# Optimization experiments

Hardware: AMD Instinct MI355X
Metric: run time of the kernel (lower is better)

The kernel has to match this reference:

```python
import jax, jax.numpy as jnp
import numpy as np

D = 64          # hidden_size
NU = 32768      # num user nodes
NI = 16384      # num item nodes
DEG = 50        # mailbox degree (== user_max_length == item_max_length)


def setup_inputs() -> dict:
    key = jax.random.key(0)
    ks = jax.random.split(key, 14)
    s = 1.0 / np.sqrt(D)
    return {
        'user_feat': jax.random.normal(ks[0], (NU, D), jnp.float32),
        'item_feat': jax.random.normal(ks[1], (NI, D), jnp.float32),
        'W_user': jax.random.normal(ks[2], (D, D), jnp.float32) * s,
        'W_item': jax.random.normal(ks[3], (D, D), jnp.float32) * s,
        'gate_u': jax.random.normal(ks[4], (D, 2 * D), jnp.float32) * s,
        'gate_i': jax.random.normal(ks[5], (D, 2 * D), jnp.float32) * s,
        'u_te': jax.random.normal(ks[6], (DEG, D), jnp.float32),
        'u_te_k': jax.random.normal(ks[7], (DEG, D), jnp.float32),
        'i_te': jax.random.normal(ks[8], (DEG, D), jnp.float32),
        'i_te_k': jax.random.normal(ks[9], (DEG, D), jnp.float32),
        'user_nbr': jax.random.randint(ks[10], (NU, DEG), 0, NI, jnp.int32),
        'item_nbr': jax.random.randint(ks[11], (NI, DEG), 0, NU, jnp.int32),
        'user_time': jax.random.randint(ks[12], (NU, DEG), 0, 1000000, jnp.int32),
        'item_time': jax.random.randint(ks[13], (NI, DEG), 0, 1000000, jnp.int32),
    }


def _orgat_att_agg(mail, dst_h, times, te, te_k, gate):
    """One reduce_func: 'orgat' long-term + 'att' short-term, gated concat.
    mail: [N, K, D] neighbor (src) embeddings; dst_h: [N, D]; times: [N, K] int.
    """
    k = times.shape[1]
    # rank of each time within the mailbox, then reversed order index
    order = jnp.argsort(jnp.argsort(times, axis=1), axis=1)
    re_order = k - order - 1                              # [N, K] in [0, K)
    scale = jnp.sqrt(jnp.asarray(mail.shape[-1], mail.dtype))
    # long-term: time-aware attention against dst embedding
    e = jnp.einsum('nkd,nd->nk', te[re_order] + mail, dst_h) / scale
    alpha = jax.nn.softmax(e, axis=1)
    h_long = jnp.einsum('nk,nkd->nd', alpha, mail + te_k[re_order])
    # short-term: attention against most-recent neighbor embedding
    last = jnp.argmax(times, axis=1)                      # [N]
    last_em = jnp.take_along_axis(mail, last[:, None, None], axis=1)[:, 0]
    e1 = jnp.einsum('nkd,nd->nk', mail, last_em) / scale
    alpha1 = jax.nn.softmax(e1, axis=1)
    h_short = jnp.einsum('nk,nkd->nd', alpha1, mail)
    return jnp.concatenate([h_long, h_short], axis=-1) @ gate.T


def reference(user_feat, item_feat, W_user, W_item, gate_u, gate_i,
              u_te, u_te_k, i_te, i_te_k,
              user_nbr, item_nbr, user_time, item_time):
    # linear projections (dropout disabled / eval mode)
    user_h = user_feat @ W_user.T
    item_h = item_feat @ W_item.T
    # item nodes aggregate from neighboring users ('by' relation)
    item_mail = user_h[item_nbr]                          # [NI, DEG, D] gather
    item_new = _orgat_att_agg(item_mail, item_h, item_time, i_te, i_te_k, gate_i)
    # user nodes aggregate from neighboring items ('pby' relation)
    user_mail = item_h[user_nbr]                          # [NU, DEG, D] gather
    user_new = _orgat_att_agg(user_mail, user_h, user_time, u_te, u_te_k, gate_u)
    # residual update with ELU against the pre-projection features
    user_out = jax.nn.elu(user_new + user_feat)
    item_out = jax.nn.elu(item_new + item_feat)
    return user_out, item_out
```

## Files before the change

### kernel.cpp

```cpp
#include <hip/hip_runtime.h>
#include <math.h>

#define NU 32768
#define NI 16384
#define DH 64
#define KK 50

typedef unsigned short ushort_t;
typedef __attribute__((ext_vector_type(8))) short  bf16x8;
typedef __attribute__((ext_vector_type(4))) float  f32x4;
typedef __attribute__((ext_vector_type(4))) unsigned int u32x4;

__device__ __forceinline__ unsigned cvtpk(float lo, float hi) {
    unsigned r;
    asm("v_cvt_pk_bf16_f32 %0, %1, %2" : "=v"(r) : "v"(lo), "v"(hi));
    return r;
}
__device__ __forceinline__ bf16x8 as_bf(u32x4 v) {
    union { u32x4 u; bf16x8 b; } x; x.u = v; return x.b;
}
__device__ __forceinline__ ushort_t bf16r(float v) {
    unsigned u = __float_as_uint(v);
    u += 0x7fffu + ((u >> 16) & 1u);
    return (ushort_t)(u >> 16);
}
__device__ __forceinline__ u32x4 pk8(const float* p) {
    float4 a = *(const float4*)p;
    float4 b = *(const float4*)(p + 4);
    u32x4 r;
    r[0] = cvtpk(a.x, a.y); r[1] = cvtpk(a.z, a.w);
    r[2] = cvtpk(b.x, b.y); r[3] = cvtpk(b.z, b.w);
    return r;
}

__global__ __launch_bounds__(256) void projprep_kernel(
    const float* __restrict__ user_feat, const float* __restrict__ item_feat,
    const float* __restrict__ W_user,    const float* __restrict__ W_item,
    const float* __restrict__ gate_u,    const float* __restrict__ gate_i,
    const float* __restrict__ u_te,      const float* __restrict__ i_te,
    const float* __restrict__ u_te_k,    const float* __restrict__ i_te_k,
    ushort_t* __restrict__ hbf_u, ushort_t* __restrict__ hbf_i,
    ushort_t* __restrict__ teA_u, ushort_t* __restrict__ teA_i,
    ushort_t* __restrict__ gA_u,  ushort_t* __restrict__ gA_i)
{
    __shared__ __align__(16) float SH[3200];
    const int b    = blockIdx.x;
    const int tid  = threadIdx.x;
    const int w    = tid >> 6;
    const int lane = tid & 63;
    const int c = lane & 15, g = lane >> 4;

    if (b < 768) {
        const bool isU = b < 512;
        const float* feat = isU ? user_feat : item_feat;
        const float* W    = isU ? W_user    : W_item;
        ushort_t*    hbf  = isU ? hbf_u     : hbf_i;
        const int    bb   = isU ? b : b - 512;

        ushort_t* WA = (ushort_t*)SH;
        for (int i = tid; i < 4096; i += 256) {
            int j = i & 7, l = (i >> 3) & 63, s = (i >> 9) & 1, mt = i >> 10;
            int row = mt * 16 + (l & 15);
            int k   = s * 32 + ((l >> 4) & 3) * 8 + j;
            WA[i] = bf16r(W[row * DH + k]);
        }
        __syncthreads();

        const int nb = bb * 64 + w * 16;
        u32x4 bf[2];
        #pragma unroll
        for (int s = 0; s < 2; ++s)
            bf[s] = pk8(feat + (size_t)(nb + c) * DH + s * 32 + g * 8);

        #pragma unroll
        for (int mt = 0; mt < 4; ++mt) {
            f32x4 acc = {0.f, 0.f, 0.f, 0.f};
            #pragma unroll
            for (int s = 0; s < 2; ++s) {
                u32x4 af = *(const u32x4*)(WA + ((mt * 2 + s) * 64 + lane) * 8);
                acc = __builtin_amdgcn_mfma_f32_16x16x32_bf16(as_bf(af), as_bf(bf[s]), acc, 0, 0, 0);
            }
            uint2 p;
            p.x = cvtpk(acc[0], acc[1]);
            p.y = cvtpk(acc[2], acc[3]);
            *(uint2*)(hbf + (size_t)(nb + c) * DH + mt * 16 + g * 4) = p;
        }
    } else {
        const int rel = b - 768;
        const float* gate = rel ? gate_i : gate_u;
        const float* te   = rel ? i_te   : u_te;
        const float* tek  = rel ? i_te_k : u_te_k;
        ushort_t* teA = rel ? teA_i : teA_u;
        ushort_t* gA  = rel ? gA_i  : gA_u;
        float* M = SH;

        {
            const int d = w * 16 + c;
            u32x4 ga[2];
            #pragma unroll
            for (int s = 0; s < 2; ++s)
                ga[s] = pk8(gate + (size_t)d * 128 + s * 32 + g * 8);
            #pragma unroll
            for (int rt = 0; rt < 4; ++rt) {
                int r = rt * 16 + c;
                const float* tr = tek + (size_t)(r < KK ? r : 0) * DH;
                f32x4 acc = {0.f, 0.f, 0.f, 0.f};
                #pragma unroll
                for (int s = 0; s < 2; ++s) {
                    u32x4 bfr = pk8(tr + s * 32 + g * 8);
                    acc = __builtin_amdgcn_mfma_f32_16x16x32_bf16(as_bf(ga[s]), as_bf(bfr), acc, 0, 0, 0);
                }
                if (r < KK) {
                    #pragma unroll
                    for (int jj = 0; jj < 4; ++jj)
                        M[(w * 16 + g * 4 + jj) * KK + r] = acc[jj];
                }
            }
        }
        __syncthreads();

        for (int i = tid; i < 4096; i += 256) {
            int j = i & 7, l = (i >> 3) & 63, s = (i >> 9) & 1, t = i >> 10;
            int r = t * 16 + (l & 15);
            int d = s * 32 + ((l >> 4) & 3) * 8 + j;
            teA[i] = bf16r(r < KK ? te[r * DH + d] : 0.f);
        }
        for (int i = tid; i < 12288; i += 256) {
            int j = i & 7, l = (i >> 3) & 63, q = i >> 9;
            int s = q % 6, mt = q / 6;
            int d = mt * 16 + (l & 15);
            int k = s * 32 + ((l >> 4) & 3) * 8 + j;
            float v = 0.f;
            if (k < 128)            v = gate[d * 128 + k];
            else if (k < 128 + KK)  v = M[d * KK + (k - 128)];
            gA[i] = bf16r(v);
        }
    }
}

__global__ __launch_bounds__(128) void agg_kernel(
    const ushort_t* __restrict__ h_src,
    const ushort_t* __restrict__ h_dst,
    const int*      __restrict__ nbr,
    const int*      __restrict__ times,
    const ushort_t* __restrict__ teA,
    ushort_t*       __restrict__ ccout)
{
    __shared__ __align__(16) float EBs[2][192];

    const int wid  = threadIdx.x >> 6;
    const int lane = threadIdx.x & 63;
    const int n    = blockIdx.x * 2 + wid;

    float* EB = EBs[wid];
    const int c = lane & 15;
    const int g = lane >> 4;

    int my_t = 0, my_nb = 0;
    if (lane < KK) {
        my_t  = times[n * KK + lane];
        my_nb = nbr[n * KK + lane];
    }

    u32x4 af[4][2];
    #pragma unroll
    for (int t = 0; t < 4; ++t) {
        int r = t * 16 + c;
        int idx = __builtin_amdgcn_ds_bpermute(r << 2, my_nb);
        const ushort_t* src = h_src + idx * DH;
        #pragma unroll
        for (int s = 0; s < 2; ++s)
            af[t][s] = *(const u32x4*)(src + s * 32 + g * 8);
    }

    int key = my_t * 64 + lane;
    int sro = 0;
    #pragma unroll
    for (int j = 0; j < KK; ++j) {
        int kj = __builtin_amdgcn_readlane(key, j);
        sro += (kj > key) ? 1 : 0;
    }

    int key2 = (lane < KK) ? (my_t * 64 + (63 - lane)) : -1;
    #pragma unroll
    for (int off = 32; off >= 1; off >>= 1) {
        int o = __shfl_xor(key2, off);
        key2 = key2 > o ? key2 : o;
    }
    const int last   = __builtin_amdgcn_readfirstlane(63 - (key2 & 63));
    const int t_last = last >> 4;
    const int c_last = last & 15;

    u32x4 fbv[2];
    {
        const ushort_t* hd = h_dst + n * DH;
        u32x4 sl0, sl1;
        if      (t_last == 0) { sl0 = af[0][0]; sl1 = af[0][1]; }
        else if (t_last == 1) { sl0 = af[1][0]; sl1 = af[1][1]; }
        else if (t_last == 2) { sl0 = af[2][0]; sl1 = af[2][1]; }
        else                  { sl0 = af[3][0]; sl1 = af[3][1]; }
        const int ba = ((lane & 48) + c_last) << 2;
        const bool is1 = (c == 1);
        #pragma unroll
        for (int s = 0; s < 2; ++s) {
            u32x4 dp = *(const u32x4*)(hd + s * 32 + g * 8);
            u32x4 sl = (s == 0) ? sl0 : sl1;
            u32x4 fb;
            #pragma unroll
            for (int u = 0; u < 4; ++u) {
                unsigned sv = (unsigned)__builtin_amdgcn_ds_bpermute(ba, (int)sl[u]);
                fb[u] = is1 ? sv : dp[u];
            }
            fbv[s] = fb;
        }
    }

    #pragma unroll
    for (int t = 0; t < 4; ++t) {
        f32x4 acc = {0.f, 0.f, 0.f, 0.f};
        #pragma unroll
        for (int s = 0; s < 2; ++s)
            acc = __builtin_amdgcn_mfma_f32_16x16x32_bf16(as_bf(af[t][s]), as_bf(fbv[s]), acc, 0, 0, 0);
        if (c < 2) {
            float* eb = EB + c * 64 + t * 16 + g * 4;
            eb[0] = acc[0]; eb[1] = acc[1]; eb[2] = acc[2]; eb[3] = acc[3];
        }
    }

    #pragma unroll
    for (int t = 0; t < 4; ++t) {
        f32x4 acc = {0.f, 0.f, 0.f, 0.f};
        #pragma unroll
        for (int s = 0; s < 2; ++s) {
            u32x4 ta = *(const u32x4*)(teA + ((t * 2 + s) * 64 + lane) * 8);
            acc = __builtin_amdgcn_mfma_f32_16x16x32_bf16(as_bf(ta), as_bf(fbv[s]), acc, 0, 0, 0);
        }
        if (c == 0) {
            float* eb = EB + 128 + t * 16 + g * 4;
            eb[0] = acc[0]; eb[1] = acc[1]; eb[2] = acc[2]; eb[3] = acc[3];
        }
    }

    float eraw  = EB[lane];
    float e1raw = EB[64 + lane];
    float tpown = EB[128 + lane];
    float tps = __uint_as_float(__builtin_amdgcn_ds_bpermute(sro << 2, __float_as_uint(tpown)));
    float e  = (lane < KK) ? (eraw + tps) * 0.125f : -INFINITY;
    float e1 = (lane < KK) ? e1raw * 0.125f        : -INFINITY;
    float m = e, m1 = e1;
    #pragma unroll
    for (int off = 32; off >= 1; off >>= 1) {
        m  = fmaxf(m,  __shfl_xor(m,  off));
        m1 = fmaxf(m1, __shfl_xor(m1, off));
    }
    float p  = (lane < KK) ? __expf(e - m)   : 0.f;
    float p1 = (lane < KK) ? __expf(e1 - m1) : 0.f;
    float s = p, s1 = p1;
    #pragma unroll
    for (int off = 32; off >= 1; off >>= 1) {
        s  += __shfl_xor(s,  off);
        s1 += __shfl_xor(s1, off);
    }
    float al  = p  * __builtin_amdgcn_rcpf(s);
    float al1 = p1 * __builtin_amdgcn_rcpf(s1);

    ushort_t* ccr = ccout + (size_t)n * 192;
    {
        int pushaddr = ((lane < KK) ? sro : lane) << 2;
        float beta = __uint_as_float(__builtin_amdgcn_ds_permute(pushaddr, __float_as_uint(al)));
        ccr[128 + lane] = bf16r(beta);
    }

    unsigned apk = cvtpk(al, al1);
    float hl = 0.f, hs = 0.f;
    #pragma unroll 10
    for (int k = 0; k < KK; ++k) {
        int idx = __builtin_amdgcn_readlane(my_nb, k);
        unsigned a = (unsigned)__builtin_amdgcn_readlane((int)apk, k);
        ushort_t u = h_src[(size_t)idx * DH + lane];
        float mv = __uint_as_float(((unsigned)u) << 16);
        hl = fmaf(__uint_as_float(a << 16), mv, hl);
        hs = fmaf(__uint_as_float(a & 0xffff0000u), mv, hs);
    }
    unsigned hp = cvtpk(hl, hs);
    ccr[lane]      = (ushort_t)hp;
    ccr[64 + lane] = (ushort_t)(hp >> 16);
}

__global__ __launch_bounds__(256) void epi_kernel(
    const ushort_t* __restrict__ cc,
    const ushort_t* __restrict__ gA,
    const float*    __restrict__ feat,
    float*          __restrict__ out)
{
    const int w    = threadIdx.x >> 6;
    const int lane = threadIdx.x & 63;
    const int c = lane & 15, g = lane >> 4;
    const int nb = (blockIdx.x * 4 + w) * 16;

    const char* ccr = (const char*)(cc + (size_t)(nb + c) * 192);
    u32x4 bb6[6];
    #pragma unroll
    for (int s = 0; s < 6; ++s)
        bb6[s] = *(const u32x4*)(ccr + s * 64 + g * 16);

    f32x4 acc[4] = {{0,0,0,0},{0,0,0,0},{0,0,0,0},{0,0,0,0}};
    #pragma unroll
    for (int mt = 0; mt < 4; ++mt)
        #pragma unroll
        for (int s = 0; s < 6; ++s) {
            u32x4 ga = *(const u32x4*)(gA + (size_t)((mt * 6 + s) * 64 + lane) * 8);
            acc[mt] = __builtin_amdgcn_mfma_f32_16x16x32_bf16(as_bf(ga), as_bf(bb6[s]), acc[mt], 0, 0, 0);
        }

    const float* fr   = feat + (size_t)(nb + c) * 64;
    float*       orow = out  + (size_t)(nb + c) * 64;
    #pragma unroll
    for (int mt = 0; mt < 4; ++mt) {
        float4 f4 = *(const float4*)(fr + mt * 16 + g * 4);
        float4 o;
        float v0 = acc[mt][0] + f4.x; o.x = v0 > 0.f ? v0 : (__expf(v0) - 1.f);
        float v1 = acc[mt][1] + f4.y; o.y = v1 > 0.f ? v1 : (__expf(v1) - 1.f);
        float v2 = acc[mt][2] + f4.z; o.z = v2 > 0.f ? v2 : (__expf(v2) - 1.f);
        float v3 = acc[mt][3] + f4.w; o.w = v3 > 0.f ? v3 : (__expf(v3) - 1.f);
        *(float4*)(orow + mt * 16 + g * 4) = o;
    }
}

extern "C" void kernel_launch(void* const* d_in, const int* in_sizes, int n_in,
                              void* d_out, int out_size, void* d_ws, size_t ws_size,
                              hipStream_t stream) {
    const float* user_feat = (const float*)d_in[0];
    const float* item_feat = (const float*)d_in[1];
    const float* W_user    = (const float*)d_in[2];
    const float* W_item    = (const float*)d_in[3];
    const float* gate_u    = (const float*)d_in[4];
    const float* gate_i    = (const float*)d_in[5];
    const float* u_te      = (const float*)d_in[6];
    const float* u_te_k    = (const float*)d_in[7];
    const float* i_te      = (const float*)d_in[8];
    const float* i_te_k    = (const float*)d_in[9];
    const int*   user_nbr  = (const int*)d_in[10];
    const int*   item_nbr  = (const int*)d_in[11];
    const int*   user_time = (const int*)d_in[12];
    const int*   item_time = (const int*)d_in[13];

    ushort_t* hbf_u = (ushort_t*)d_ws;
    ushort_t* hbf_i = hbf_u + NU * DH;
    ushort_t* teA_u = hbf_i + NI * DH;
    ushort_t* teA_i = teA_u + 4096;
    ushort_t* gA_u  = teA_i + 4096;
    ushort_t* gA_i  = gA_u + 12288;
    ushort_t* cc_i  = gA_i + 12288;
    ushort_t* cc_u  = cc_i + (size_t)NI * 192;

    float* user_out = (float*)d_out;
    float* item_out = user_out + NU * DH;

    hipLaunchKernelGGL(projprep_kernel, dim3(770), dim3(256), 0, stream,
                       user_feat, item_feat, W_user, W_item, gate_u, gate_i,
                       u_te, i_te, u_te_k, i_te_k,
                       hbf_u, hbf_i, teA_u, teA_i, gA_u, gA_i);
    hipLaunchKernelGGL(agg_kernel, dim3(NI / 2), dim3(128), 0, stream,
                       hbf_u, hbf_i, item_nbr, item_time, teA_i, cc_i);
    hipLaunchKernelGGL(agg_kernel, dim3(NU / 2), dim3(128), 0, stream,
                       hbf_i, hbf_u, user_nbr, user_time, teA_u, cc_u);
    hipLaunchKernelGGL(epi_kernel, dim3(NI / 64), dim3(256), 0, stream,
                       cc_i, gA_i, item_feat, item_out);
    hipLaunchKernelGGL(epi_kernel, dim3(NU / 64), dim3(256), 0, stream,
                       cc_u, gA_u, user_feat, user_out);
}
```

Before: 126.4 us.

## Merge item/user launches and prefetch all mailbox rows before aggregation

Merges the item and user aggregation kernels into one grid, and does the same for the two epilogue kernels, selecting pointers by block index. This removes launch gaps and tail effects between the dependent launches. The 50 per-lane mailbox gathers are now issued up front into a register array, so they overlap with the ranking and softmax work instead of sitting in the final reduction loop. Index math also switches to 32-bit unsigned offsets. The cost is higher register pressure, which may lower occupancy.

```diff
diff --git a/kernel.cpp b/kernel.cpp
--- a/kernel.cpp
+++ b/kernel.cpp
@@ -139,18 +139,26 @@
 }
 
 __global__ __launch_bounds__(128) void agg_kernel(
-    const ushort_t* __restrict__ h_src,
-    const ushort_t* __restrict__ h_dst,
-    const int*      __restrict__ nbr,
-    const int*      __restrict__ times,
-    const ushort_t* __restrict__ teA,
-    ushort_t*       __restrict__ ccout)
+    const ushort_t* __restrict__ hbf_u, const ushort_t* __restrict__ hbf_i,
+    const int* __restrict__ item_nbr,  const int* __restrict__ item_time,
+    const int* __restrict__ user_nbr,  const int* __restrict__ user_time,
+    const ushort_t* __restrict__ teA_u, const ushort_t* __restrict__ teA_i,
+    ushort_t* __restrict__ cc_i, ushort_t* __restrict__ cc_u)
 {
     __shared__ __align__(16) float EBs[2][192];
 
     const int wid  = threadIdx.x >> 6;
     const int lane = threadIdx.x & 63;
-    const int n    = blockIdx.x * 2 + wid;
+    const int b    = blockIdx.x;
+    const bool isU = b >= (NI / 2);
+
+    const ushort_t* h_src = isU ? hbf_i : hbf_u;
+    const ushort_t* h_dst = isU ? hbf_u : hbf_i;
+    const int*      nbr   = isU ? user_nbr  : item_nbr;
+    const int*      times = isU ? user_time : item_time;
+    const ushort_t* teA   = isU ? teA_u : teA_i;
+    ushort_t*       ccout = isU ? cc_u  : cc_i;
+    const int n = (isU ? b - NI / 2 : b) * 2 + wid;
 
     float* EB = EBs[wid];
     const int c = lane & 15;
@@ -158,8 +166,15 @@
 
     int my_t = 0, my_nb = 0;
     if (lane < KK) {
-        my_t  = times[n * KK + lane];
-        my_nb = nbr[n * KK + lane];
+        my_t  = times[(unsigned)(n * KK) + lane];
+        my_nb = nbr[(unsigned)(n * KK) + lane];
+    }
+
+    unsigned mv[KK];
+    #pragma unroll
+    for (int k = 0; k < KK; ++k) {
+        int idx = __builtin_amdgcn_readlane(my_nb, k);
+        mv[k] = (unsigned)h_src[(unsigned)(idx * DH) + lane];
     }
 
     u32x4 af[4][2];
@@ -167,7 +182,7 @@
     for (int t = 0; t < 4; ++t) {
         int r = t * 16 + c;
         int idx = __builtin_amdgcn_ds_bpermute(r << 2, my_nb);
-        const ushort_t* src = h_src + idx * DH;
+        const ushort_t* src = h_src + (unsigned)(idx * DH);
         #pragma unroll
         for (int s = 0; s < 2; ++s)
             af[t][s] = *(const u32x4*)(src + s * 32 + g * 8);
@@ -193,7 +208,7 @@
 
     u32x4 fbv[2];
     {
-        const ushort_t* hd = h_dst + n * DH;
+        const ushort_t* hd = h_dst + (unsigned)(n * DH);
         u32x4 sl0, sl1;
         if      (t_last == 0) { sl0 = af[0][0]; sl1 = af[0][1]; }
         else if (t_last == 1) { sl0 = af[1][0]; sl1 = af[1][1]; }
@@ -264,7 +279,7 @@
     float al  = p  * __builtin_amdgcn_rcpf(s);
     float al1 = p1 * __builtin_amdgcn_rcpf(s1);
 
-    ushort_t* ccr = ccout + (size_t)n * 192;
+    ushort_t* ccr = ccout + (unsigned)(n * 192);
     {
         int pushaddr = ((lane < KK) ? sro : lane) << 2;
         float beta = __uint_as_float(__builtin_amdgcn_ds_permute(pushaddr, __float_as_uint(al)));
@@ -273,14 +288,12 @@
 
     unsigned apk = cvtpk(al, al1);
     float hl = 0.f, hs = 0.f;
-    #pragma unroll 10
+    #pragma unroll
     for (int k = 0; k < KK; ++k) {
-        int idx = __builtin_amdgcn_readlane(my_nb, k);
         unsigned a = (unsigned)__builtin_amdgcn_readlane((int)apk, k);
-        ushort_t u = h_src[(size_t)idx * DH + lane];
-        float mv = __uint_as_float(((unsigned)u) << 16);
-        hl = fmaf(__uint_as_float(a << 16), mv, hl);
-        hs = fmaf(__uint_as_float(a & 0xffff0000u), mv, hs);
+        float mvf = __uint_as_float(mv[k] << 16);
+        hl = fmaf(__uint_as_float(a << 16), mvf, hl);
+        hs = fmaf(__uint_as_float(a & 0xffff0000u), mvf, hs);
     }
     unsigned hp = cvtpk(hl, hs);
     ccr[lane]      = (ushort_t)hp;
@@ -288,15 +301,23 @@
 }
 
 __global__ __launch_bounds__(256) void epi_kernel(
-    const ushort_t* __restrict__ cc,
-    const ushort_t* __restrict__ gA,
-    const float*    __restrict__ feat,
-    float*          __restrict__ out)
+    const ushort_t* __restrict__ cc_i, const ushort_t* __restrict__ cc_u,
+    const ushort_t* __restrict__ gA_i, const ushort_t* __restrict__ gA_u,
+    const float* __restrict__ item_feat, const float* __restrict__ user_feat,
+    float* __restrict__ item_out, float* __restrict__ user_out)
 {
+    const int b = blockIdx.x;
+    const bool isU = b >= (NI / 64);
+    const ushort_t* cc   = isU ? cc_u : cc_i;
+    const ushort_t* gA   = isU ? gA_u : gA_i;
+    const float*    feat = isU ? user_feat : item_feat;
+    float*          out  = isU ? user_out  : item_out;
+    const int bb = isU ? b - NI / 64 : b;
+
     const int w    = threadIdx.x >> 6;
     const int lane = threadIdx.x & 63;
     const int c = lane & 15, g = lane >> 4;
-    const int nb = (blockIdx.x * 4 + w) * 16;
+    const int nb = bb * 64 + w * 16;
 
     const char* ccr = (const char*)(cc + (size_t)(nb + c) * 192);
     u32x4 bb6[6];
@@ -361,12 +382,10 @@
                        user_feat, item_feat, W_user, W_item, gate_u, gate_i,
                        u_te, i_te, u_te_k, i_te_k,
                        hbf_u, hbf_i, teA_u, teA_i, gA_u, gA_i);
-    hipLaunchKernelGGL(agg_kernel, dim3(NI / 2), dim3(128), 0, stream,
-                       hbf_u, hbf_i, item_nbr, item_time, teA_i, cc_i);
-    hipLaunchKernelGGL(agg_kernel, dim3(NU / 2), dim3(128), 0, stream,
-                       hbf_i, hbf_u, user_nbr, user_time, teA_u, cc_u);
-    hipLaunchKernelGGL(epi_kernel, dim3(NI / 64), dim3(256), 0, stream,
-                       cc_i, gA_i, item_feat, item_out);
-    hipLaunchKernelGGL(epi_kernel, dim3(NU / 64), dim3(256), 0, stream,
-                       cc_u, gA_u, user_feat, user_out);
-}
+    hipLaunchKernelGGL(agg_kernel, dim3(NI / 2 + NU / 2), dim3(128), 0, stream,
+                       hbf_u, hbf_i, item_nbr, item_time, user_nbr, user_time,
+                       teA_u, teA_i, cc_i, cc_u);
+    hipLaunchKernelGGL(epi_kernel, dim3(NI / 64 + NU / 64), dim3(256), 0, stream,
+                       cc_i, cc_u, gA_i, gA_u, item_feat, user_feat,
+                       item_out, user_out);
+}
```

Result: slower. 146.8 us (+16.2%).
